# Kernel tuning notes

Hardware: AMD Instinct MI355X
Metric: run time of the kernel (lower is better)

## Reference

```python
import jax, jax.numpy as jnp
import numpy as np

THRESHOLD = 1.0
B, T, I, H = 128, 512, 512, 1024

def setup_inputs() -> dict:
    key = jax.random.key(0)
    ks = jax.random.split(key, 6)
    s = lambda k, shape, fan: jax.random.normal(k, shape, dtype=jnp.float32) * (1.0 / np.sqrt(fan))
    return {
        "x": jax.random.normal(ks[0], (B, T, I), dtype=jnp.float32),
        "Wi": s(ks[1], (H, I), I),
        "bi": s(ks[2], (H,), I),
        "Wh": s(ks[3], (H, H), H),
        "bh": s(ks[4], (H,), H),
        "h0": jnp.zeros((1, H), dtype=jnp.float32),
    }

def reference(x, Wi, bi, Wh, bh, h0):
    # hidden_init tiled to batch
    hidden = jnp.tile(h0, (x.shape[0], 1))  # [B, H]
    # Precompute input projection for all timesteps in one big GEMM: [B, T, H]
    xin = jnp.einsum('bti,hi->bth', x, Wi) + bi
    xin_t = jnp.swapaxes(xin, 0, 1)  # [T, B, H] for scan

    def step(h, xt):
        pre = h + xt + jnp.dot(h, Wh.T) + bh  # hidden + i2h(x) + h2h(hidden)
        h_new = jnp.minimum(jax.nn.relu(pre), THRESHOLD)
        return h_new, h_new

    hidden, outs = jax.lax.scan(step, hidden, xin_t)
    rnn_out = jnp.swapaxes(outs, 0, 1)  # [B, T, H]
    return rnn_out, hidden
```

## Files before the change

### kernel.cpp

```cpp
#include <hip/hip_runtime.h>
#include <cstddef>

#define B_ 128
#define T_ 512
#define I_ 512
#define H_ 1024
#define TH_ (T_ * H_)
#define PSTR 257
#define LDSN (32 * PSTR)

__global__ __launch_bounds__(256) void k_input_gemm(
    const float* __restrict__ A, const float* __restrict__ W,
    const float* __restrict__ bi, float* __restrict__ C)
{
    const int nb = blockIdx.x;
    const int mb = blockIdx.y;
    const int tid = threadIdx.x;
    const int tx = tid & 15;
    const int ty = tid >> 4;

    __shared__ float As[16][132];
    __shared__ float Ws[16][132];

    float acc[8][8];
#pragma unroll
    for (int i = 0; i < 8; ++i)
#pragma unroll
        for (int j = 0; j < 8; ++j) acc[i][j] = 0.f;

    const float* Ab = A + (size_t)mb * 128 * I_;
    const float* Wb = W + (size_t)nb * 128 * I_;

    for (int kt = 0; kt < I_; kt += 16) {
        {
            const int r = tid >> 2;
            const int kq = (tid & 3) * 4;
            float4 v0 = *(const float4*)(Ab + (size_t)r * I_ + kt + kq);
            float4 v1 = *(const float4*)(Ab + (size_t)(r + 64) * I_ + kt + kq);
            As[kq + 0][r] = v0.x; As[kq + 1][r] = v0.y;
            As[kq + 2][r] = v0.z; As[kq + 3][r] = v0.w;
            As[kq + 0][r + 64] = v1.x; As[kq + 1][r + 64] = v1.y;
            As[kq + 2][r + 64] = v1.z; As[kq + 3][r + 64] = v1.w;
            float4 w0 = *(const float4*)(Wb + (size_t)r * I_ + kt + kq);
            float4 w1 = *(const float4*)(Wb + (size_t)(r + 64) * I_ + kt + kq);
            Ws[kq + 0][r] = w0.x; Ws[kq + 1][r] = w0.y;
            Ws[kq + 2][r] = w0.z; Ws[kq + 3][r] = w0.w;
            Ws[kq + 0][r + 64] = w1.x; Ws[kq + 1][r + 64] = w1.y;
            Ws[kq + 2][r + 64] = w1.z; Ws[kq + 3][r + 64] = w1.w;
        }
        __syncthreads();

#pragma unroll
        for (int kk = 0; kk < 16; ++kk) {
            float4 a0 = *(const float4*)&As[kk][ty * 8];
            float4 a1 = *(const float4*)&As[kk][ty * 8 + 4];
            float4 b0 = *(const float4*)&Ws[kk][tx * 8];
            float4 b1 = *(const float4*)&Ws[kk][tx * 8 + 4];
            float av[8] = {a0.x, a0.y, a0.z, a0.w, a1.x, a1.y, a1.z, a1.w};
            float bv[8] = {b0.x, b0.y, b0.z, b0.w, b1.x, b1.y, b1.z, b1.w};
#pragma unroll
            for (int i = 0; i < 8; ++i)
#pragma unroll
                for (int j = 0; j < 8; ++j) acc[i][j] += av[i] * bv[j];
        }
        __syncthreads();
    }

    const int n0 = nb * 128 + tx * 8;
    float4 bv0 = *(const float4*)(bi + n0);
    float4 bv1 = *(const float4*)(bi + n0 + 4);
#pragma unroll
    for (int i = 0; i < 8; ++i) {
        const size_t m = (size_t)mb * 128 + ty * 8 + i;
        float4 c0, c1;
        c0.x = acc[i][0] + bv0.x; c0.y = acc[i][1] + bv0.y;
        c0.z = acc[i][2] + bv0.z; c0.w = acc[i][3] + bv0.w;
        c1.x = acc[i][4] + bv1.x; c1.y = acc[i][5] + bv1.y;
        c1.z = acc[i][6] + bv1.z; c1.w = acc[i][7] + bv1.w;
        *(float4*)(C + m * H_ + n0) = c0;
        *(float4*)(C + m * H_ + n0 + 4) = c1;
    }
}

__global__ __launch_bounds__(256, 2) void k_rnn(
    const float* __restrict__ Wh, const float* __restrict__ bh,
    const float* __restrict__ h0, float* __restrict__ out,
    unsigned* __restrict__ bar)
{
    __shared__ float lds[LDSN];

    const int bx = blockIdx.x;
    const int bt = bx & 15;
    const int nt = bx >> 4;
    const int m0 = bt * 8;
    const int n0 = nt * 32;
    const int tid = threadIdx.x;
    const int c = tid & 7;
    const int s = tid >> 3;

    float4 wreg[4][8];
#pragma unroll
    for (int j = 0; j < 4; ++j) {
        const float* wp = Wh + (size_t)(n0 + c * 4 + j) * H_ + s * 4;
#pragma unroll
        for (int jj = 0; jj < 8; ++jj)
            wreg[j][jj] = *(const float4*)(wp + jj * 128);
    }

    const int r  = tid >> 5;
    const int nl = tid & 31;
    const float bh1 = bh[n0 + nl];
    unsigned* grp = bar + bt * 32;

    for (int t = 0; t < T_; ++t) {
        const float* hb; size_t rstr;
        if (t == 0) { hb = h0; rstr = 0; }
        else        { hb = out + (size_t)(t - 1) * H_; rstr = TH_; }

        unsigned long long stg[16];
#pragma unroll
        for (int i = 0; i < 16; ++i) {
            const int f = i * 256 + tid;
            const int p = f >> 9;
            const int col2 = f & 511;
            const unsigned long long* gp = (const unsigned long long*)
                (hb + (size_t)(m0 + p) * rstr + (size_t)col2 * 2);
            stg[i] = __hip_atomic_load(gp, __ATOMIC_RELAXED,
                                       __HIP_MEMORY_SCOPE_SYSTEM);
        }
        const size_t g0 = (size_t)(m0 + r) * TH_ + (size_t)t * H_ + n0 + nl;
        const float xin1 = out[g0];

#pragma unroll
        for (int i = 0; i < 16; ++i) {
            const int f = i * 256 + tid;
            const int p = f >> 9;
            const int col2 = f & 511;
            *(unsigned long long*)&lds[p * 1024 + col2 * 2] = stg[i];
        }
        __syncthreads();

        const float hp1 = lds[r * 1024 + n0 + nl];

        float acc[8][4];
#pragma unroll
        for (int m = 0; m < 8; ++m)
#pragma unroll
            for (int j = 0; j < 4; ++j) acc[m][j] = 0.f;

#pragma unroll
        for (int m = 0; m < 8; ++m) {
#pragma unroll
            for (int jj = 0; jj < 8; ++jj) {
                float4 h4 = *(const float4*)&lds[m * 1024 + jj * 128 + s * 4];
#pragma unroll
                for (int j = 0; j < 4; ++j) {
                    acc[m][j] += h4.x * wreg[j][jj].x;
                    acc[m][j] += h4.y * wreg[j][jj].y;
                    acc[m][j] += h4.z * wreg[j][jj].z;
                    acc[m][j] += h4.w * wreg[j][jj].w;
                }
            }
        }
        __syncthreads();

#pragma unroll
        for (int m = 0; m < 8; ++m)
#pragma unroll
            for (int j = 0; j < 4; ++j)
                lds[PSTR * s + m * 32 + c * 4 + j] = acc[m][j];
        __syncthreads();

        float red = 0.f;
#pragma unroll
        for (int g = 0; g < 32; ++g)
            red += lds[PSTR * g + tid];

        const float res = fminf(fmaxf(hp1 + xin1 + red + bh1, 0.f), 1.f);
        __hip_atomic_store(out + g0, res, __ATOMIC_RELAXED,
                           __HIP_MEMORY_SCOPE_SYSTEM);
        if (t == T_ - 1) {
            out[(size_t)B_ * TH_ + (size_t)(m0 + r) * H_ + n0 + nl] = res;
        }

        asm volatile("s_waitcnt vmcnt(0)" ::: "memory");
        __syncthreads();
        if (tid == 0) {
            __hip_atomic_store(&grp[nt], (unsigned)(t + 1), __ATOMIC_RELAXED,
                               __HIP_MEMORY_SCOPE_SYSTEM);
        }
        if (tid < 64) {
            const unsigned tgt = (unsigned)(t + 1);
            for (;;) {
                unsigned v = __hip_atomic_load(&grp[tid & 31], __ATOMIC_RELAXED,
                                               __HIP_MEMORY_SCOPE_SYSTEM);
                if (__all(v >= tgt)) break;
                __builtin_amdgcn_s_sleep(1);
            }
        }
        __syncthreads();
    }
}

extern "C" void kernel_launch(void* const* d_in, const int* in_sizes, int n_in,
                              void* d_out, int out_size, void* d_ws, size_t ws_size,
                              hipStream_t stream)
{
    const float* x  = (const float*)d_in[0];
    const float* Wi = (const float*)d_in[1];
    const float* bi = (const float*)d_in[2];
    const float* Wh = (const float*)d_in[3];
    const float* bh = (const float*)d_in[4];
    const float* h0 = (const float*)d_in[5];
    float* out = (float*)d_out;
    unsigned* bar = (unsigned*)d_ws;

    const size_t zn = ws_size < 2048 ? ws_size : 2048;
    hipMemsetAsync(d_ws, 0, zn, stream);

    k_input_gemm<<<dim3(8, 512), 256, 0, stream>>>(x, Wi, bi, out);

    k_rnn<<<dim3(512), dim3(256), 0, stream>>>(Wh, bh, h0, out, bar);
}
```

Baseline: 5.574 ms.

## Replace per-step group barrier with offset-tagged values in double-buffered exchange

Each block publishes its hidden values into a double-buffered workspace with a step-dependent additive offset. Consumers poll the values until all fall within the expected offset range, then subtract the offset. This removes the separate flag store, the vmcnt wait and the spin barrier each timestep, so data arrival itself acts as synchronization. It depends on hidden values staying in [0,1] and adds retry loads while data is not yet ready.

```diff
diff --git a/kernel.cpp b/kernel.cpp
--- a/kernel.cpp
+++ b/kernel.cpp
@@ -8,6 +8,7 @@
 #define TH_ (T_ * H_)
 #define PSTR 257
 #define LDSN (32 * PSTR)
+#define XBN (B_ * H_)
 
 __global__ __launch_bounds__(256) void k_input_gemm(
     const float* __restrict__ A, const float* __restrict__ W,
@@ -82,10 +83,14 @@
     }
 }
 
+__device__ __forceinline__ float ofs_of(int t) {
+    return 8.0f + 4.0f * (float)((t >> 1) & 1);
+}
+
 __global__ __launch_bounds__(256, 2) void k_rnn(
     const float* __restrict__ Wh, const float* __restrict__ bh,
     const float* __restrict__ h0, float* __restrict__ out,
-    unsigned* __restrict__ bar)
+    float* __restrict__ xbuf)
 {
     __shared__ float lds[LDSN];
 
@@ -110,33 +115,71 @@
     const int r  = tid >> 5;
     const int nl = tid & 31;
     const float bh1 = bh[n0 + nl];
-    unsigned* grp = bar + bt * 32;
 
     for (int t = 0; t < T_; ++t) {
-        const float* hb; size_t rstr;
-        if (t == 0) { hb = h0; rstr = 0; }
-        else        { hb = out + (size_t)(t - 1) * H_; rstr = TH_; }
-
-        unsigned long long stg[16];
-#pragma unroll
-        for (int i = 0; i < 16; ++i) {
-            const int f = i * 256 + tid;
-            const int p = f >> 9;
-            const int col2 = f & 511;
-            const unsigned long long* gp = (const unsigned long long*)
-                (hb + (size_t)(m0 + p) * rstr + (size_t)col2 * 2);
-            stg[i] = __hip_atomic_load(gp, __ATOMIC_RELAXED,
-                                       __HIP_MEMORY_SCOPE_SYSTEM);
-        }
         const size_t g0 = (size_t)(m0 + r) * TH_ + (size_t)t * H_ + n0 + nl;
         const float xin1 = out[g0];
 
-#pragma unroll
-        for (int i = 0; i < 16; ++i) {
-            const int f = i * 256 + tid;
-            const int p = f >> 9;
-            const int col2 = f & 511;
-            *(unsigned long long*)&lds[p * 1024 + col2 * 2] = stg[i];
+        if (t == 0) {
+#pragma unroll
+            for (int i = 0; i < 16; ++i) {
+                const int f = i * 256 + tid;
+                const int p = f >> 9;
+                const int col2 = f & 511;
+                const unsigned long long v =
+                    *(const unsigned long long*)(h0 + (size_t)col2 * 2);
+                *(unsigned long long*)&lds[p * 1024 + col2 * 2] = v;
+            }
+        } else {
+            const unsigned long long* xb = (const unsigned long long*)
+                (xbuf + (size_t)((t - 1) & 1) * XBN);
+            const float osub = ofs_of(t - 1);
+            const float olo = osub - 0.5f;
+            const float ohi = osub + 1.5f;
+
+            unsigned long long stg[16];
+#pragma unroll
+            for (int i = 0; i < 16; ++i) {
+                const int f = i * 256 + tid;
+                const int p = f >> 9;
+                const int col2 = f & 511;
+                stg[i] = __hip_atomic_load(&xb[(size_t)(m0 + p) * 512 + col2],
+                                           __ATOMIC_RELAXED,
+                                           __HIP_MEMORY_SCOPE_SYSTEM);
+            }
+            for (;;) {
+                unsigned bad = 0;
+#pragma unroll
+                for (int i = 0; i < 16; ++i) {
+                    const float lo = __uint_as_float((unsigned)(stg[i] & 0xffffffffull));
+                    const float hi = __uint_as_float((unsigned)(stg[i] >> 32));
+                    const bool ok = (lo >= olo) & (lo <= ohi) &
+                                    (hi >= olo) & (hi <= ohi);
+                    if (!ok) bad |= (1u << i);
+                }
+                if (!bad) break;
+#pragma unroll
+                for (int i = 0; i < 16; ++i) {
+                    if (bad & (1u << i)) {
+                        const int f = i * 256 + tid;
+                        const int p = f >> 9;
+                        const int col2 = f & 511;
+                        stg[i] = __hip_atomic_load(&xb[(size_t)(m0 + p) * 512 + col2],
+                                                   __ATOMIC_RELAXED,
+                                                   __HIP_MEMORY_SCOPE_SYSTEM);
+                    }
+                }
+            }
+#pragma unroll
+            for (int i = 0; i < 16; ++i) {
+                const int f = i * 256 + tid;
+                const int p = f >> 9;
+                const int col2 = f & 511;
+                float lo = __uint_as_float((unsigned)(stg[i] & 0xffffffffull)) - osub;
+                float hi = __uint_as_float((unsigned)(stg[i] >> 32)) - osub;
+                float2 v; v.x = lo; v.y = hi;
+                *(float2*)&lds[p * 1024 + col2 * 2] = v;
+            }
         }
         __syncthreads();
 
@@ -177,27 +220,15 @@
             red += lds[PSTR * g + tid];
 
         const float res = fminf(fmaxf(hp1 + xin1 + red + bh1, 0.f), 1.f);
-        __hip_atomic_store(out + g0, res, __ATOMIC_RELAXED,
-                           __HIP_MEMORY_SCOPE_SYSTEM);
+        out[g0] = res;
         if (t == T_ - 1) {
             out[(size_t)B_ * TH_ + (size_t)(m0 + r) * H_ + n0 + nl] = res;
-        }
-
-        asm volatile("s_waitcnt vmcnt(0)" ::: "memory");
-        __syncthreads();
-        if (tid == 0) {
-            __hip_atomic_store(&grp[nt], (unsigned)(t + 1), __ATOMIC_RELAXED,
-                               __HIP_MEMORY_SCOPE_SYSTEM);
-        }
-        if (tid < 64) {
-            const unsigned tgt = (unsigned)(t + 1);
-            for (;;) {
-                unsigned v = __hip_atomic_load(&grp[tid & 31], __ATOMIC_RELAXED,
-                                               __HIP_MEMORY_SCOPE_SYSTEM);
-                if (__all(v >= tgt)) break;
-                __builtin_amdgcn_s_sleep(1);
-            }
-        }
+        } else {
+            __hip_atomic_store(
+                xbuf + (size_t)(t & 1) * XBN + (size_t)(m0 + r) * H_ + n0 + nl,
+                res + ofs_of(t), __ATOMIC_RELAXED, __HIP_MEMORY_SCOPE_SYSTEM);
+        }
+
         __syncthreads();
     }
 }
@@ -213,12 +244,13 @@
     const float* bh = (const float*)d_in[4];
     const float* h0 = (const float*)d_in[5];
     float* out = (float*)d_out;
-    unsigned* bar = (unsigned*)d_ws;
-
-    const size_t zn = ws_size < 2048 ? ws_size : 2048;
+    float* xbuf = (float*)d_ws;
+
+    const size_t need = (size_t)2 * XBN * sizeof(float);
+    const size_t zn = ws_size < need ? ws_size : need;
     hipMemsetAsync(d_ws, 0, zn, stream);
 
     k_input_gemm<<<dim3(8, 512), 256, 0, stream>>>(x, Wi, bi, out);
 
-    k_rnn<<<dim3(512), dim3(256), 0, stream>>>(Wh, bh, h0, out, bar);
-}
+    k_rnn<<<dim3(512), dim3(256), 0, stream>>>(Wh, bh, h0, out, xbuf);
+}
```

Result: no change. 5.556 ms (-0.3%).
